# Performance work log

Measured on AMD Instinct MI355X. Metric: run time of the kernel, lower is better.

Reference implementation:

```python
import jax, jax.numpy as jnp
import numpy as np
import math

H = 16
D_ATTN = 64
D_MID = 64
D_X = 1024
D_Z = 1024
D_OUT = 1024
B = 2
L_X = 2048
L_Z = 2048
MINUS_INFINITY = -1000000.0

def _xavier(key, shape):
    fan_in, fan_out = shape
    limit = math.sqrt(6.0 / (fan_in + fan_out))
    return jax.random.uniform(key, shape, jnp.float32, -limit, limit)

def setup_inputs() -> dict:
    key = jax.random.key(0)
    ks = jax.random.split(key, 8)
    primary = jax.random.normal(ks[0], (B, L_X, D_X), jnp.float32)
    context = jax.random.normal(ks[1], (B, L_Z, D_Z), jnp.float32)
    padding_mask = jnp.ones((B, L_Z), jnp.int32)
    # causal attention mask (b, l_x, l_z)
    attention_mask = jnp.broadcast_to(
        jnp.tril(jnp.ones((L_X, L_Z), jnp.int32))[None], (B, L_X, L_Z))
    W_qs = _xavier(ks[2], (D_X, H * D_ATTN))
    W_ks = _xavier(ks[3], (D_Z, H * D_ATTN))
    W_vs = _xavier(ks[4], (D_Z, H * D_MID))
    W_o = _xavier(ks[5], (H * D_MID, D_OUT))
    b_o = jnp.zeros((D_OUT,), jnp.float32)
    return {"primary": primary, "context": context,
            "padding_mask": padding_mask, "attention_mask": attention_mask,
            "W_qs": W_qs, "W_ks": W_ks, "W_vs": W_vs, "W_o": W_o, "b_o": b_o}

def reference(primary, context, padding_mask, attention_mask, W_qs, W_ks, W_vs, W_o, b_o):
    b, l_x, _ = primary.shape
    l_z = context.shape[1]
    # QKV projections, split into heads (head-major columns)
    q = (primary @ W_qs).reshape(b, l_x, H, D_ATTN).transpose(0, 2, 1, 3)  # (b,h,l_x,d_attn)
    k = (context @ W_ks).reshape(b, l_z, H, D_ATTN).transpose(0, 2, 1, 3)  # (b,h,l_z,d_attn)
    v = (context @ W_vs).reshape(b, l_z, H, D_MID).transpose(0, 2, 1, 3)   # (b,h,l_z,d_mid)
    scores = jnp.einsum('bhxd,bhzd->bhxz', q, k) / math.sqrt(D_ATTN)
    # combined mask: attention_mask AND padding_mask, broadcast over heads
    mask = (attention_mask * padding_mask[:, None, :])[:, None]  # (b,1,l_x,l_z)
    scores = jnp.where(mask == 0, MINUS_INFINITY, scores)
    attn = jax.nn.softmax(scores, axis=-1)
    out = jnp.einsum('bhxz,bhzm->bhxm', attn, v)  # (b,h,l_x,d_mid)
    out = out.transpose(0, 2, 1, 3).reshape(b, l_x, H * D_MID)
    return out @ W_o + b_o
```

## Files before the change

### kernel.cpp

```cpp
#include <hip/hip_runtime.h>

#define NB 2
#define LX 2048
#define LZ 2048
#define HH 16
#define DA 64
#define DM 64
#define HD 1024
#define KVS 2048
#define MINF  -1000000.0f
#define QSC   0.1803368801f
#define DTHR  8.0f

typedef __attribute__((ext_vector_type(8))) short short8;
typedef __attribute__((ext_vector_type(4))) float f32x4;

static __device__ __forceinline__ ushort f2bf(float f) {
    union { float f; uint32_t u; } c; c.f = f;
    return (ushort)((c.u + 0x7FFFu + ((c.u >> 16) & 1u)) >> 16);
}

static __device__ __forceinline__ float bf2f(ushort u) {
    union { uint32_t u; float f; } c; c.u = (uint32_t)u << 16;
    return c.f;
}

static __device__ __forceinline__ uint32_t cvtpk(float lo, float hi) {
    uint32_t r;
    asm("v_cvt_pk_bf16_f32 %0, %1, %2" : "=v"(r) : "v"(lo), "v"(hi));
    return r;
}

#define GL16(g, l) __builtin_amdgcn_global_load_lds( \
    (const __attribute__((address_space(1))) void*)(g), \
    (__attribute__((address_space(3))) void*)(l), 16, 0, 0)

__global__ __launch_bounds__(256) void prep(
    const float* __restrict__ pA, const float* __restrict__ pB,
    ushort* __restrict__ oA, ushort* __restrict__ oB,
    const float* __restrict__ W0, const float* __restrict__ W1,
    const float* __restrict__ W2, const float* __restrict__ W3,
    ushort* __restrict__ T0, ushort* __restrict__ T1,
    ushort* __restrict__ T2, ushort* __restrict__ T3,
    const int* __restrict__ amask, const int* __restrict__ pmask,
    int* __restrict__ cls)
{
    const int fid = blockIdx.x;
    const int t = threadIdx.x;
    if (fid < 8192) {
        const int i = fid * 256 + t;
        const float* in = (i < 1048576) ? pA : pB;
        ushort* out = (i < 1048576) ? oA : oB;
        const int j = i & 1048575;
        float4 v = ((const float4*)in)[j];
        ushort4 o;
        o.x = f2bf(v.x); o.y = f2bf(v.y); o.z = f2bf(v.z); o.w = f2bf(v.w);
        ((ushort4*)out)[j] = o;
    } else if (fid < 9216) {
        __shared__ ushort Ls[64][72];
        const int id2 = fid - 8192;
        const int zz = id2 >> 8, rem = id2 & 255;
        const float* W = (zz == 0) ? W0 : (zz == 1) ? W1 : (zz == 2) ? W2 : W3;
        ushort* Wt = (zz == 0) ? T0 : (zz == 1) ? T1 : (zz == 2) ? T2 : T3;
        const int n0 = (rem & 15) * 64, k0 = (rem >> 4) * 64;
        const int rr = t >> 4, c4 = (t & 15) * 4;
        #pragma unroll
        for (int i = 0; i < 4; ++i) {
            const int r = rr + i * 16;
            float4 v = *(const float4*)&W[(size_t)(k0 + r) * 1024 + n0 + c4];
            Ls[c4 + 0][r] = f2bf(v.x);
            Ls[c4 + 1][r] = f2bf(v.y);
            Ls[c4 + 2][r] = f2bf(v.z);
            Ls[c4 + 3][r] = f2bf(v.w);
        }
        __syncthreads();
        const int n = t >> 2, kc = (t & 3) * 16;
        *(short8*)&Wt[(size_t)(n0 + n) * 1024 + k0 + kc]     = *(const short8*)&Ls[n][kc];
        *(short8*)&Wt[(size_t)(n0 + n) * 1024 + k0 + kc + 8] = *(const short8*)&Ls[n][kc + 8];
    } else {
        const int bid = fid - 9216;
        const int b = bid >> 10, xb = (bid >> 5) & 31, zb = bid & 31;
        int andv = 1, orv = 0;
        #pragma unroll
        for (int i = 0; i < 16; ++i) {
            const int e = t + i * 256;
            const int r = e >> 6, z = e & 63;
            const int m = amask[((size_t)b * LX + xb * 64 + r) * LZ + zb * 64 + z];
            const int p = pmask[(size_t)b * LZ + zb * 64 + z];
            const int v = (m != 0) & (p != 0);
            andv &= v; orv |= v;
        }
        __shared__ int sa[256];
        __shared__ int so[256];
        sa[t] = andv; so[t] = orv;
        __syncthreads();
        for (int s = 128; s > 0; s >>= 1) {
            if (t < s) { sa[t] &= sa[t + s]; so[t] |= so[t + s]; }
            __syncthreads();
        }
        if (t == 0) cls[bid] = so[0] ? (sa[0] ? 1 : 2) : 0;
    }
}

__global__ __launch_bounds__(256) void gemm_qkv(
    const ushort* __restrict__ Pb, const ushort* __restrict__ Cb,
    const ushort* __restrict__ Wqt, const ushort* __restrict__ Wkvt,
    ushort* __restrict__ Qb, ushort* __restrict__ KV)
{
    const int bx = blockIdx.x;
    const bool isQ = bx < 8;
    const ushort* A  = isQ ? Pb : Cb;
    const ushort* Bt = isQ ? Wqt : Wkvt;
    ushort* Cout = isQ ? Qb : KV;
    const int n0 = (isQ ? bx : bx - 8) * 128;
    const int ostr = isQ ? 1024 : KVS;
    const float osc = isQ ? QSC : 1.0f;

    __shared__ ushort As[128 * 32];
    __shared__ ushort Bs[128 * 32];
    const int t = threadIdx.x;
    const int w = t >> 6, l = t & 63, lr = l & 15, lg = l >> 4;
    const int wr = w >> 1, wc = w & 1;
    const int m0 = blockIdx.y * 128;

    const int c0 = t, c1 = t + 256;
    const ushort* a0 = &A[(size_t)(m0 + (c0 >> 2)) * 1024 + (c0 & 3) * 8];
    const ushort* a1 = &A[(size_t)(m0 + (c1 >> 2)) * 1024 + (c1 & 3) * 8];
    const ushort* b0 = &Bt[(size_t)(n0 + (c0 >> 2)) * 1024 + (c0 & 3) * 8];
    const ushort* b1 = &Bt[(size_t)(n0 + (c1 >> 2)) * 1024 + (c1 & 3) * 8];
    ushort* lA0 = &As[w * 512];
    ushort* lA1 = &As[(4 + w) * 512];
    ushort* lB0 = &Bs[w * 512];
    ushort* lB1 = &Bs[(4 + w) * 512];

    f32x4 acc[4][4];
    #pragma unroll
    for (int i = 0; i < 4; ++i)
        #pragma unroll
        for (int j = 0; j < 4; ++j) acc[i][j] = 0.f;

    for (int k0 = 0; k0 < 1024; k0 += 32) {
        __syncthreads();
        GL16(a0 + k0, lA0);
        GL16(a1 + k0, lA1);
        GL16(b0 + k0, lB0);
        GL16(b1 + k0, lB1);
        __syncthreads();
        short8 af[4], bf[4];
        #pragma unroll
        for (int mi = 0; mi < 4; ++mi)
            af[mi] = *(const short8*)&As[(wr * 64 + mi * 16 + lr) * 32 + lg * 8];
        #pragma unroll
        for (int nj = 0; nj < 4; ++nj)
            bf[nj] = *(const short8*)&Bs[(wc * 64 + nj * 16 + lr) * 32 + lg * 8];
        #pragma unroll
        for (int mi = 0; mi < 4; ++mi)
            #pragma unroll
            for (int nj = 0; nj < 4; ++nj)
                acc[mi][nj] = __builtin_amdgcn_mfma_f32_16x16x32_bf16(
                    af[mi], bf[nj], acc[mi][nj], 0, 0, 0);
    }

    const int row0 = m0 + wr * 64, col0 = n0 + wc * 64;
    #pragma unroll
    for (int mi = 0; mi < 4; ++mi)
        #pragma unroll
        for (int nj = 0; nj < 4; ++nj) {
            const int col = col0 + nj * 16 + lr;
            #pragma unroll
            for (int r = 0; r < 4; ++r) {
                const int row = row0 + mi * 16 + lg * 4 + r;
                Cout[(size_t)row * ostr + col] = f2bf(acc[mi][nj][r] * osc);
            }
        }
}

__global__ __launch_bounds__(256, 4) void attn_mfma(
    const ushort* __restrict__ Qg, const ushort* __restrict__ KVg,
    const int* __restrict__ amask, const int* __restrict__ pmask,
    const int* __restrict__ cls, ushort* __restrict__ Op,
    float2* __restrict__ ml)
{
    __shared__ ushort Ks[64 * 64];
    __shared__ ushort Vt[64 * 64];

    const int t = threadIdx.x, w = t >> 6, l = t & 63, lr = l & 15, lg = l >> 4;
    const int flat = blockIdx.x + 16 * (blockIdx.y + 16 * blockIdx.z);
    const int xcd = flat & 7, ii = flat >> 3;
    const int g = xcd + 8 * (ii >> 4);
    const int pp = ii & 15;
    const int h = g & 15, bs = g >> 4;
    const int b = bs & 1, sKV = bs >> 1;
    const uint32_t halfm = sKV ? 0xAAAAAAAAu : 0x55555555u;

    const int qb0 = pp, qb1 = 31 - pp;
    const int qw0 = qb0 * 64 + w * 16, qw1 = qb1 * 64 + w * 16;
    const int cv0 = cls[b * 1024 + qb0 * 32 + (l & 31)];
    const int cv1 = cls[b * 1024 + qb1 * 32 + (l & 31)];
    const uint32_t act0 = (uint32_t)__ballot(cv0 != 0) & halfm;
    const uint32_t mix0 = (uint32_t)__ballot(cv0 == 2) & halfm;
    const uint32_t act1 = (uint32_t)__ballot(cv1 != 0) & halfm;
    const uint32_t mix1 = (uint32_t)__ballot(cv1 == 2) & halfm;

    short8 qfA[2], qfB[2];
    #pragma unroll
    for (int ks = 0; ks < 2; ++ks) {
        qfA[ks] = *(const short8*)&Qg[(size_t)(b * LX + qw0 + lr) * HD
                                      + h * DA + ks * 32 + lg * 8];
        qfB[ks] = *(const short8*)&Qg[(size_t)(b * LX + qw1 + lr) * HD
                                      + h * DA + ks * 32 + lg * 8];
    }

    float mrunA = -1e30f, lrunA = 0.f, mrunB = -1e30f, lrunB = 0.f;
    f32x4 oA[4], oB[4];
    #pragma unroll
    for (int mj = 0; mj < 4; ++mj) { oA[mj] = 0.f; oB[mj] = 0.f; }

    const int zs0 = t >> 3, zs1 = 32 + (t >> 3);
    const int cs = t & 7;
    const int gc0 = (cs ^ (zs0 & 7)) << 3;
    ushort* kdst0 = &Ks[w * 512];
    ushort* kdst1 = &Ks[2048 + w * 512];
    const size_t kbase = (size_t)(b * LZ) * KVS + h * DA;
    const int vz = (t >> 3) * 2, vc = (t & 7) * 8;

#define STRIP_COMPUTE(QW, QF, MRUN, LRUN, OO, MIXBIT)                          \
    do {                                                                       \
        f32x4 s[4];                                                           \
        __builtin_amdgcn_s_setprio(1);                                        \
        _Pragma("unroll")                                                      \
        for (int nj = 0; nj < 4; ++nj) {                                      \
            const int row = nj * 16 + lr;                                     \
            const int sw = row & 7;                                           \
            const short8 kf0 = *(const short8*)&Ks[row * 64 + ((lg ^ sw) << 3)];\
            const short8 kf1 = *(const short8*)&Ks[row * 64 + (((4 + lg) ^ sw) << 3)];\
            f32x4 z4 = 0.f;                                                   \
            z4 = __builtin_amdgcn_mfma_f32_16x16x32_bf16(kf0, (QF)[0], z4, 0, 0, 0);\
            z4 = __builtin_amdgcn_mfma_f32_16x16x32_bf16(kf1, (QF)[1], z4, 0, 0, 0);\
            s[nj] = z4;                                                       \
        }                                                                      \
        __builtin_amdgcn_s_setprio(0);                                        \
        if (MIXBIT) {                                                          \
            const size_t arow = (size_t)(b * LX + (QW) + lr) * LZ + z0;       \
            _Pragma("unroll")                                                  \
            for (int nj = 0; nj < 4; ++nj)                                    \
                _Pragma("unroll")                                              \
                for (int r = 0; r < 4; ++r) {                                 \
                    const int z = nj * 16 + lg * 4 + r;                       \
                    const int ok = (amask[arow + z] != 0) & (pmask[b * LZ + z0 + z] != 0);\
                    if (!ok) s[nj][r] = MINF;                                 \
                }                                                              \
        }                                                                      \
        {                                                                      \
            float pm = s[0][0];                                               \
            _Pragma("unroll")                                                  \
            for (int nj = 0; nj < 4; ++nj)                                    \
                _Pragma("unroll")                                              \
                for (int r = 0; r < 4; ++r) pm = fmaxf(pm, s[nj][r]);         \
            pm = fmaxf(pm, __shfl_xor(pm, 16));                               \
            pm = fmaxf(pm, __shfl_xor(pm, 32));                               \
            if (__any(pm > (MRUN) + DTHR)) {                                  \
                const float mn = fmaxf((MRUN), pm);                           \
                const float al = exp2f((MRUN) - mn);                          \
                (MRUN) = mn;                                                  \
                (LRUN) *= al;                                                 \
                _Pragma("unroll")                                              \
                for (int r = 0; r < 4; ++r) {                                 \
                    const float alq = __shfl(al, (lg << 2) + r);              \
                    _Pragma("unroll")                                          \
                    for (int mj = 0; mj < 4; ++mj) (OO)[mj][r] *= alq;        \
                }                                                              \
            }                                                                  \
            _Pragma("unroll")                                                  \
            for (int nj = 0; nj < 4; ++nj)                                    \
                _Pragma("unroll")                                              \
                for (int r = 0; r < 4; ++r) {                                 \
                    const float p = exp2f(s[nj][r] - (MRUN));                 \
                    s[nj][r] = p;                                             \
                    (LRUN) += p;                                              \
                }                                                              \
        }                                                                      \
        short8 pa[2];                                                         \
        {                                                                      \
            uint32_t pk01[4], pk23[4];                                        \
            _Pragma("unroll")                                                  \
            for (int nj = 0; nj < 4; ++nj) {                                  \
                pk01[nj] = cvtpk(s[nj][0], s[nj][1]);                         \
                pk23[nj] = cvtpk(s[nj][2], s[nj][3]);                         \
            }                                                                  \
            _Pragma("unroll")                                                  \
            for (int ks = 0; ks < 2; ++ks) {                                  \
                union { uint32_t d[4]; short8 v; } u;                         \
                u.d[0] = pk01[2 * ks];                                        \
                u.d[1] = pk23[2 * ks];                                        \
                u.d[2] = pk01[2 * ks + 1];                                    \
                u.d[3] = pk23[2 * ks + 1];                                    \
                pa[ks] = u.v;                                                 \
            }                                                                  \
        }                                                                      \
        __builtin_amdgcn_s_setprio(1);                                        \
        _Pragma("unroll")                                                      \
        for (int mj = 0; mj < 4; ++mj) {                                      \
            const int m_ = mj * 16 + lr;                                      \
            const int xr = (m_ ^ (m_ >> 3)) & 7;                              \
            const int czb = lg >> 1;                                          \
            const int zo = (lg & 1) * 4;                                      \
            _Pragma("unroll")                                                  \
            for (int ks = 0; ks < 2; ++ks) {                                  \
                const int clo = (ks * 4 + czb) ^ xr;                          \
                const int chi = (ks * 4 + 2 + czb) ^ xr;                      \
                const uint2 lo = *(const uint2*)&Vt[m_ * 64 + ((clo & 7) << 3) + zo];\
                const uint2 hi = *(const uint2*)&Vt[m_ * 64 + ((chi & 7) << 3) + zo];\
                union { uint32_t d[4]; short8 v; } u;                         \
                u.d[0] = lo.x; u.d[1] = lo.y; u.d[2] = hi.x; u.d[3] = hi.y;   \
                (OO)[mj] = __builtin_amdgcn_mfma_f32_16x16x32_bf16(pa[ks], u.v, (OO)[mj], 0, 0, 0);\
            }                                                                  \
        }                                                                      \
        __builtin_amdgcn_s_setprio(0);                                        \
    } while (0)

    uint32_t remU = act0 | act1;
    while (remU) {
        const int zb = __builtin_ctz(remU);
        remU &= remU - 1;
        const int z0 = zb * 64;

        __syncthreads();
        GL16(&KVg[kbase + (size_t)(z0 + zs0) * KVS + gc0], kdst0);
        GL16(&KVg[kbase + (size_t)(z0 + zs1) * KVS + gc0], kdst1);
        {
            const ushort* vp = &KVg[(size_t)(b * LZ + z0 + vz) * KVS + 1024 + h * DM + vc];
            short8 v0 = *(const short8*)vp;
            short8 v1 = *(const short8*)(vp + KVS);
            const int zc = vz >> 3, zo = vz & 7;
            #pragma unroll
            for (int j = 0; j < 8; ++j) {
                const int m = vc + j;
                const int idx = m * 64 + (((zc ^ m ^ (m >> 3)) & 7) << 3) + zo;
                *(uint32_t*)&Vt[idx] =
                    (uint32_t)(ushort)v0[j] | ((uint32_t)(ushort)v1[j] << 16);
            }
        }
        __syncthreads();

        if ((act0 >> zb) & 1)
            STRIP_COMPUTE(qw0, qfA, mrunA, lrunA, (&oA[0] - 0), ((mix0 >> zb) & 1));
        if ((act1 >> zb) & 1)
            STRIP_COMPUTE(qw1, qfB, mrunB, lrunB, (&oB[0] - 0), ((mix1 >> zb) & 1));
    }
#undef STRIP_COMPUTE

    lrunA += __shfl_xor(lrunA, 16);
    lrunA += __shfl_xor(lrunA, 32);
    lrunB += __shfl_xor(lrunB, 16);
    lrunB += __shfl_xor(lrunB, 32);
    if (l < 16) {
        ml[(size_t)((sKV * NB + b) * HH + h) * LX + qw0 + l] = make_float2(mrunA, lrunA);
        ml[(size_t)((sKV * NB + b) * HH + h) * LX + qw1 + l] = make_float2(mrunB, lrunB);
    }
    const size_t ob0 = (size_t)((sKV * NB + b) * LX + qw0) * HD + h * DM;
    const size_t ob1 = (size_t)((sKV * NB + b) * LX + qw1) * HD + h * DM;
    #pragma unroll
    for (int r = 0; r < 4; ++r)
        #pragma unroll
        for (int mj = 0; mj < 4; ++mj) {
            Op[ob0 + (size_t)((lg << 2) + r) * HD + mj * 16 + lr] = f2bf(oA[mj][r]);
            Op[ob1 + (size_t)((lg << 2) + r) * HD + mj * 16 + lr] = f2bf(oB[mj][r]);
        }
}

__global__ __launch_bounds__(256) void gemm_out_fused(
    const ushort* __restrict__ Op, const float2* __restrict__ ml,
    const ushort* __restrict__ Bt, const float* __restrict__ bias,
    float* __restrict__ Cout)
{
    __shared__ ushort As[64 * 32];
    __shared__ ushort Bs[128 * 32];
    __shared__ float2 Wl[64][17];
    const int t = threadIdx.x;
    const int w = t >> 6, l = t & 63, lr = l & 15, lg = l >> 4;
    const int wr = w >> 1, wc = w & 1;
    const int n0 = blockIdx.x * 128, m0 = blockIdx.y * 64;

    {
        const int e = t * 4;
        #pragma unroll
        for (int j = 0; j < 4; ++j) {
            const int rl = (e + j) >> 4, hh = (e + j) & 15;
            const int ra = m0 + rl;
            const int bb = ra >> 11, xx = ra & 2047;
            const float2 a0 = ml[(size_t)(bb * HH + hh) * LX + xx];
            const float2 a1 = ml[(size_t)((NB + bb) * HH + hh) * LX + xx];
            const float M = fmaxf(a0.x, a1.x);
            const float w0 = exp2f(a0.x - M), w1 = exp2f(a1.x - M);
            const float inv = 1.f / fmaxf(a0.y * w0 + a1.y * w1, 1e-37f);
            Wl[rl][hh] = make_float2(w0 * inv, w1 * inv);
        }
    }
    __syncthreads();

    const int ra = m0 + (t >> 2), ka = (t & 3) * 8;
    const ushort* p0 = &Op[(size_t)ra * HD + ka];
    const ushort* p1 = p0 + (size_t)NB * LX * HD;
    const ushort* b0 = &Bt[(size_t)(n0 + (t >> 2)) * 1024 + ka];
    const ushort* b1 = &Bt[(size_t)(n0 + 64 + (t >> 2)) * 1024 + ka];
    ushort* lB0 = &Bs[w * 512];
    ushort* lB1 = &Bs[(4 + w) * 512];

    f32x4 acc[2][4];
    #pragma unroll
    for (int i = 0; i < 2; ++i)
        #pragma unroll
        for (int j = 0; j < 4; ++j) acc[i][j] = 0.f;

    for (int k0 = 0; k0 < 1024; k0 += 32) {
        const short8 q0 = *(const short8*)(p0 + k0);
        const short8 q1 = *(const short8*)(p1 + k0);
        const float2 wv = Wl[t >> 2][(k0 + ka) >> 6];
        union { ushort d[8]; short8 v; } av;
        #pragma unroll
        for (int j = 0; j < 8; ++j)
            av.d[j] = f2bf(bf2f((ushort)q0[j]) * wv.x + bf2f((ushort)q1[j]) * wv.y);
        __syncthreads();
        *(short8*)&As[t * 8] = av.v;
        GL16(b0 + k0, lB0);
        GL16(b1 + k0, lB1);
        __syncthreads();
        short8 af[2], bf[4];
        #pragma unroll
        for (int mi = 0; mi < 2; ++mi)
            af[mi] = *(const short8*)&As[(wr * 32 + mi * 16 + lr) * 32 + lg * 8];
        #pragma unroll
        for (int nj = 0; nj < 4; ++nj)
            bf[nj] = *(const short8*)&Bs[(wc * 64 + nj * 16 + lr) * 32 + lg * 8];
        #pragma unroll
        for (int mi = 0; mi < 2; ++mi)
            #pragma unroll
            for (int nj = 0; nj < 4; ++nj)
                acc[mi][nj] = __builtin_amdgcn_mfma_f32_16x16x32_bf16(
                    af[mi], bf[nj], acc[mi][nj], 0, 0, 0);
    }

    const int row0 = m0 + wr * 32, col0 = n0 + wc * 64;
    #pragma unroll
    for (int mi = 0; mi < 2; ++mi)
        #pragma unroll
        for (int nj = 0; nj < 4; ++nj) {
            const int col = col0 + nj * 16 + lr;
            #pragma unroll
            for (int r = 0; r < 4; ++r) {
                const int row = row0 + mi * 16 + lg * 4 + r;
                Cout[(size_t)row * 1024 + col] = acc[mi][nj][r] + bias[col];
            }
        }
}

extern "C" void kernel_launch(void* const* d_in, const int* in_sizes, int n_in,
                              void* d_out, int out_size, void* d_ws, size_t ws_size,
                              hipStream_t stream)
{
    const float* primary = (const float*)d_in[0];
    const float* context = (const float*)d_in[1];
    const int*   pmask   = (const int*)d_in[2];
    const int*   amask   = (const int*)d_in[3];
    const float* Wq      = (const float*)d_in[4];
    const float* Wk      = (const float*)d_in[5];
    const float* Wv      = (const float*)d_in[6];
    const float* Wo      = (const float*)d_in[7];
    const float* bo      = (const float*)d_in[8];
    float* out = (float*)d_out;

    char* w8 = (char*)d_ws;
    ushort* Pb  = (ushort*)(w8 + 0);
    ushort* Cb  = (ushort*)(w8 + 8388608);
    ushort* Qb  = (ushort*)(w8 + 16777216);
    ushort* KV  = (ushort*)(w8 + 25165824);
    ushort* Wqt = (ushort*)(w8 + 50331648);
    ushort* Wkt = (ushort*)(w8 + 52428800);
    ushort* Wvt = (ushort*)(w8 + 54525952);
    ushort* Wot = (ushort*)(w8 + 56623104);
    int*    clsp = (int*)(w8 + 58720256);
    ushort* Op   = Pb;
    float2* mlp  = (float2*)Wqt;

    prep<<<11264, 256, 0, stream>>>(primary, context, Pb, Cb,
                                    Wq, Wk, Wv, Wo, Wqt, Wkt, Wvt, Wot,
                                    amask, pmask, clsp);
    gemm_qkv<<<dim3(24, 32), 256, 0, stream>>>(Pb, Cb, Wqt, Wkt, Qb, KV);
    attn_mfma<<<dim3(16, 16, 4), 256, 0, stream>>>(Qb, KV, amask, pmask, clsp, Op, mlp);
    gemm_out_fused<<<dim3(8, 64), 256, 0, stream>>>(Op, mlp, Wot, bo, out);
}
```

Measured before the change: 131.6 us.

## Emit V transposed from QKV GEMM and load it with direct LDS copies

The QKV projection GEMM now writes K and V to separate buffers. V is transposed through shared memory and stored as a (head*dim, batch*seq) matrix. The attention kernel can then load V tiles with the same async global-to-LDS copies used for K, replacing per-thread register loads and a scalar scatter into the swizzled Vt tile. The cost is an extra LDS round trip and two barriers in the GEMM epilogue for the V blocks.

```diff
diff --git a/kernel.cpp b/kernel.cpp
--- a/kernel.cpp
+++ b/kernel.cpp
@@ -7,7 +7,6 @@
 #define DA 64
 #define DM 64
 #define HD 1024
-#define KVS 2048
 #define MINF  -1000000.0f
 #define QSC   0.1803368801f
 #define DTHR  8.0f
@@ -105,19 +104,20 @@
 __global__ __launch_bounds__(256) void gemm_qkv(
     const ushort* __restrict__ Pb, const ushort* __restrict__ Cb,
     const ushort* __restrict__ Wqt, const ushort* __restrict__ Wkvt,
-    ushort* __restrict__ Qb, ushort* __restrict__ KV)
+    ushort* __restrict__ Qb, ushort* __restrict__ Kb, ushort* __restrict__ VT)
 {
+    __shared__ ushort sh[8704];
+    ushort* As = sh;
+    ushort* Bs = sh + 4096;
+
     const int bx = blockIdx.x;
     const bool isQ = bx < 8;
+    const bool isV = bx >= 16;
     const ushort* A  = isQ ? Pb : Cb;
     const ushort* Bt = isQ ? Wqt : Wkvt;
-    ushort* Cout = isQ ? Qb : KV;
     const int n0 = (isQ ? bx : bx - 8) * 128;
-    const int ostr = isQ ? 1024 : KVS;
     const float osc = isQ ? QSC : 1.0f;
 
-    __shared__ ushort As[128 * 32];
-    __shared__ ushort Bs[128 * 32];
     const int t = threadIdx.x;
     const int w = t >> 6, l = t & 63, lr = l & 15, lg = l >> 4;
     const int wr = w >> 1, wc = w & 1;
@@ -161,25 +161,52 @@
                     af[mi], bf[nj], acc[mi][nj], 0, 0, 0);
     }
 
-    const int row0 = m0 + wr * 64, col0 = n0 + wc * 64;
-    #pragma unroll
-    for (int mi = 0; mi < 4; ++mi)
-        #pragma unroll
-        for (int nj = 0; nj < 4; ++nj) {
-            const int col = col0 + nj * 16 + lr;
+    if (!isV) {
+        ushort* Cout = isQ ? Qb : Kb;
+        const int row0 = m0 + wr * 64, col0 = n0 + wc * 64;
+        #pragma unroll
+        for (int mi = 0; mi < 4; ++mi)
             #pragma unroll
-            for (int r = 0; r < 4; ++r) {
-                const int row = row0 + mi * 16 + lg * 4 + r;
-                Cout[(size_t)row * ostr + col] = f2bf(acc[mi][nj][r] * osc);
+            for (int nj = 0; nj < 4; ++nj) {
+                const int col = col0 + nj * 16 + lr;
+                #pragma unroll
+                for (int r = 0; r < 4; ++r) {
+                    const int row = row0 + mi * 16 + lg * 4 + r;
+                    Cout[(size_t)row * 1024 + col] = f2bf(acc[mi][nj][r] * osc);
+                }
             }
-        }
+    } else {
+        #pragma unroll
+        for (int h2 = 0; h2 < 2; ++h2) {
+            __syncthreads();
+            if (wc == h2) {
+                #pragma unroll
+                for (int nj = 0; nj < 4; ++nj)
+                    #pragma unroll
+                    for (int mi = 0; mi < 4; ++mi)
+                        #pragma unroll
+                        for (int r = 0; r < 4; ++r)
+                            sh[(nj * 16 + lr) * 136 + wr * 64 + mi * 16 + lg * 4 + r]
+                                = f2bf(acc[mi][nj][r]);
+            }
+            __syncthreads();
+            const int vcl = t >> 2, seg = t & 3;
+            const int vcol = (n0 - 1024) + h2 * 64 + vcl;
+            ushort* dst = &VT[(size_t)vcol * 4096 + m0 + seg * 32];
+            const ushort* srcl = &sh[vcl * 136 + seg * 32];
+            *(short8*)(dst + 0)  = *(const short8*)(srcl + 0);
+            *(short8*)(dst + 8)  = *(const short8*)(srcl + 8);
+            *(short8*)(dst + 16) = *(const short8*)(srcl + 16);
+            *(short8*)(dst + 24) = *(const short8*)(srcl + 24);
+        }
+    }
 }
 
 __global__ __launch_bounds__(256, 4) void attn_mfma(
-    const ushort* __restrict__ Qg, const ushort* __restrict__ KVg,
-    const int* __restrict__ amask, const int* __restrict__ pmask,
-    const int* __restrict__ cls, ushort* __restrict__ Op,
-    float2* __restrict__ ml)
+    const ushort* __restrict__ Qg, const ushort* __restrict__ Kb,
+    const ushort* __restrict__ VTg, const int* __restrict__ amask,
+    const int* __restrict__ pmask, const int* __restrict__ cls,
+    ushort* __restrict__ Op, float2* __restrict__ ml)
 {
     __shared__ ushort Ks[64 * 64];
     __shared__ ushort Vt[64 * 64];
@@ -221,8 +248,17 @@
     const int gc0 = (cs ^ (zs0 & 7)) << 3;
     ushort* kdst0 = &Ks[w * 512];
     ushort* kdst1 = &Ks[2048 + w * 512];
-    const size_t kbase = (size_t)(b * LZ) * KVS + h * DA;
-    const int vz = (t >> 3) * 2, vc = (t & 7) * 8;
+    const size_t kbase = (size_t)(b * LZ) * 1024 + h * DA;
+    const int vm0 = t >> 3, vm1 = 32 + (t >> 3);
+    const int vq = t & 7;
+    const int vf0 = (vm0 ^ (vm0 >> 3)) & 7;
+    const int vf1 = (vm1 ^ (vm1 >> 3)) & 7;
+    const int voff0 = ((vq ^ vf0) << 3);
+    const int voff1 = ((vq ^ vf1) << 3);
+    ushort* vdst0 = &Vt[w * 512];
+    ushort* vdst1 = &Vt[2048 + w * 512];
+    const size_t vtb0 = (size_t)(h * 64 + vm0) * 4096 + b * LZ;
+    const size_t vtb1 = (size_t)(h * 64 + vm1) * 4096 + b * LZ;
 
 #define STRIP_COMPUTE(QW, QF, MRUN, LRUN, OO, MIXBIT)                          \
     do {                                                                       \
@@ -326,21 +362,10 @@
         const int z0 = zb * 64;
 
         __syncthreads();
-        GL16(&KVg[kbase + (size_t)(z0 + zs0) * KVS + gc0], kdst0);
-        GL16(&KVg[kbase + (size_t)(z0 + zs1) * KVS + gc0], kdst1);
-        {
-            const ushort* vp = &KVg[(size_t)(b * LZ + z0 + vz) * KVS + 1024 + h * DM + vc];
-            short8 v0 = *(const short8*)vp;
-            short8 v1 = *(const short8*)(vp + KVS);
-            const int zc = vz >> 3, zo = vz & 7;
-            #pragma unroll
-            for (int j = 0; j < 8; ++j) {
-                const int m = vc + j;
-                const int idx = m * 64 + (((zc ^ m ^ (m >> 3)) & 7) << 3) + zo;
-                *(uint32_t*)&Vt[idx] =
-                    (uint32_t)(ushort)v0[j] | ((uint32_t)(ushort)v1[j] << 16);
-            }
-        }
+        GL16(&Kb[kbase + (size_t)(z0 + zs0) * 1024 + gc0], kdst0);
+        GL16(&Kb[kbase + (size_t)(z0 + zs1) * 1024 + gc0], kdst1);
+        GL16(&VTg[vtb0 + z0 + voff0], vdst0);
+        GL16(&VTg[vtb1 + z0 + voff1], vdst1);
         __syncthreads();
 
         if ((act0 >> zb) & 1)
@@ -474,7 +499,8 @@
     ushort* Pb  = (ushort*)(w8 + 0);
     ushort* Cb  = (ushort*)(w8 + 8388608);
     ushort* Qb  = (ushort*)(w8 + 16777216);
-    ushort* KV  = (ushort*)(w8 + 25165824);
+    ushort* Kb  = (ushort*)(w8 + 25165824);
+    ushort* VT  = (ushort*)(w8 + 33554432);
     ushort* Wqt = (ushort*)(w8 + 50331648);
     ushort* Wkt = (ushort*)(w8 + 52428800);
     ushort* Wvt = (ushort*)(w8 + 54525952);
@@ -486,7 +512,7 @@
     prep<<<11264, 256, 0, stream>>>(primary, context, Pb, Cb,
                                     Wq, Wk, Wv, Wo, Wqt, Wkt, Wvt, Wot,
                                     amask, pmask, clsp);
-    gemm_qkv<<<dim3(24, 32), 256, 0, stream>>>(Pb, Cb, Wqt, Wkt, Qb, KV);
-    attn_mfma<<<dim3(16, 16, 4), 256, 0, stream>>>(Qb, KV, amask, pmask, clsp, Op, mlp);
+    gemm_qkv<<<dim3(24, 32), 256, 0, stream>>>(Pb, Cb, Wqt, Wkt, Qb, Kb, VT);
+    attn_mfma<<<dim3(16, 16, 4), 256, 0, stream>>>(Qb, Kb, VT, amask, pmask, clsp, Op, mlp);
     gemm_out_fused<<<dim3(8, 64), 256, 0, stream>>>(Op, mlp, Wot, bo, out);
 }
```

Measured after the change: 145.0 us. 1.1x slower.
